# Kernel tuning notes

Measured on AMD Instinct MI355X. Metric: run time of the kernel, lower is better.

The kernel has to match this reference:

```python
import jax, jax.numpy as jnp
import numpy as np

NUM_HEADS = 32
NUM_KV_HEADS = 8
HEAD_DIM = 128
SCALE = 1.0 / np.sqrt(128.0)
B = 8          # num sequences
LQ = 1024 // 8 # new (query) tokens per sequence
PAGE_SIZE = 16


def setup_inputs() -> dict:
    key = jax.random.key(0)
    ks = jax.random.split(key, 5)
    q = jax.random.normal(ks[0], (B * LQ, NUM_HEADS * HEAD_DIM), dtype=jnp.float32)
    k = jax.random.normal(ks[1], (B * LQ, NUM_KV_HEADS * HEAD_DIM), dtype=jnp.float32)
    v = jax.random.normal(ks[2], (B * LQ, NUM_KV_HEADS * HEAD_DIM), dtype=jnp.float32)
    k_cache = jax.random.normal(ks[3], (1024, PAGE_SIZE, NUM_KV_HEADS, HEAD_DIM), dtype=jnp.float32)
    v_cache = jax.random.normal(ks[4], (1024, PAGE_SIZE, NUM_KV_HEADS, HEAD_DIM), dtype=jnp.float32)
    page_tables = jnp.arange(8 * 128, dtype=jnp.int64).reshape(8, 128)  # distinct pages per seq
    return {"q": q, "k": k, "v": v, "k_cache": k_cache, "v_cache": v_cache,
            "page_tables": page_tables, "ctx_len": 2048, "block_size": 32}


def reference(q, k, v, k_cache, v_cache, page_tables, ctx_len, block_size):
    nh, nkvh, hd = NUM_HEADS, NUM_KV_HEADS, HEAD_DIM
    group = nh // nkvh
    # split flat token dim into [B, Lq]
    qs = q.reshape(B, LQ, nh, hd)
    k_new = k.reshape(B, LQ, nkvh, hd)
    v_new = v.reshape(B, LQ, nkvh, hd)
    # paged gather of cached context: [B, n_pages, P, nkvh, hd] -> [B, ctx_len, nkvh, hd]
    k_ctx = k_cache[page_tables].reshape(B, ctx_len, nkvh, hd)
    v_ctx = v_cache[page_tables].reshape(B, ctx_len, nkvh, hd)
    k_full = jnp.concatenate([k_ctx, k_new], axis=1)  # [B, ctx_len+Lq, nkvh, hd]
    v_full = jnp.concatenate([v_ctx, v_new], axis=1)
    # GQA: repeat kv heads to match query heads (repeat_interleave over head dim)
    k_rep = jnp.repeat(k_full, group, axis=2)  # [B, K, nh, hd]
    v_rep = jnp.repeat(v_full, group, axis=2)
    scores = jnp.einsum('bqhd,bkhd->bhqk', qs, k_rep) * SCALE  # [B, nh, Lq, K]
    # diffusion block-causal mask over the new-token region; cache region fully visible
    qi = jnp.arange(LQ)
    abs_q = ctx_len + qi
    abs_k_new = ctx_len + jnp.arange(LQ)
    block_ends = (abs_q // block_size + 1) * block_size
    new_mask = abs_k_new[None, :] < block_ends[:, None]            # [Lq, Lq]
    cache_mask = jnp.ones((LQ, ctx_len), dtype=bool)
    mask = jnp.concatenate([cache_mask, new_mask], axis=1)         # [Lq, ctx_len+Lq]
    neg = jnp.finfo(scores.dtype).min
    scores = jnp.where(mask[None, None, :, :], scores, neg)
    probs = jax.nn.softmax(scores, axis=-1)
    out = jnp.einsum('bhqk,bkhd->bqhd', probs, v_rep)  # [B, Lq, nh, hd]
    return out.reshape(B * LQ, nh * hd).astype(q.dtype)
```

## Files before the change

### kernel.cpp

```cpp
#include <hip/hip_runtime.h>
#include <math.h>

#define NH 32
#define NKVH 8
#define GRP 4
#define HD 128
#define LQB 128
#define PTSTRIDE 128
#define KVROW (NKVH * HD)
#define QK_SCALE 0.08838834764831845f

typedef __attribute__((ext_vector_type(8))) __bf16 bf16x8;
typedef __attribute__((ext_vector_type(4))) __bf16 bf16x4;
typedef __attribute__((ext_vector_type(4))) float f32x4;

#define KS_BYTES 8192
#define VT_BYTES 10240
#define KS_OFF(b) ((b) * KS_BYTES)
#define VT_OFF(b) (2 * KS_BYTES + (b) * VT_BYTES)

static __device__ __forceinline__ bf16x8 cvt8s(const float* __restrict__ p, float s) {
    const f32x4 a = *reinterpret_cast<const f32x4*>(p);
    const f32x4 b = *reinterpret_cast<const f32x4*>(p + 4);
    bf16x8 r;
    r[0] = (__bf16)(a[0] * s); r[1] = (__bf16)(a[1] * s);
    r[2] = (__bf16)(a[2] * s); r[3] = (__bf16)(a[3] * s);
    r[4] = (__bf16)(b[0] * s); r[5] = (__bf16)(b[1] * s);
    r[6] = (__bf16)(b[2] * s); r[7] = (__bf16)(b[3] * s);
    return r;
}

__global__ __launch_bounds__(256, 2)
void attn_fwd(const float* __restrict__ Q,
              const float* __restrict__ Kn,
              const float* __restrict__ Vn,
              const float* __restrict__ Kc,
              const float* __restrict__ Vc,
              const int* __restrict__ PT,
              const int* __restrict__ CTX,
              float* __restrict__ O)
{
    __shared__ __align__(16) unsigned char smem[2 * KS_BYTES + 2 * VT_BYTES];

    const int ctx  = CTX[0];
    const int tid  = (int)threadIdx.x;
    const int wave = tid >> 6;
    const int lane = tid & 63;
    const int low  = lane & 15;
    const int hi   = lane >> 4;

    const int bid   = (int)blockIdx.x;
    const int kvh   = bid & 7;
    const int b     = (bid >> 3) & 7;
    const int qtile = bid >> 6;
    const int head  = kvh * GRP + wave;
    const int q0    = qtile * 16;

    const int qtok = b * LQB + q0 + low;
    const float* qrow = Q + (size_t)qtok * (NH * HD) + head * HD;

    bf16x8 qf[4];
    #pragma unroll
    for (int c = 0; c < 4; ++c) qf[c] = cvt8s(qrow + 32 * c + 8 * hi, QK_SCALE);

    f32x4 acc[8];
    #pragma unroll
    for (int c = 0; c < 8; ++c) acc[c] = (f32x4){0.f, 0.f, 0.f, 0.f};
    float mrun = -1e30f, lrun = 0.f;

    const int skey = tid >> 3;
    const int sc8  = tid & 7;
    const int kxr  = (skey & 7) << 4;
    const int vdc  = tid >> 3;
    const int vkq  = tid & 7;

    f32x4 kr[4], vr[4];

    const int nsteps = (ctx >> 5) + (q0 >> 5) + 1;

    auto issue_loads = [&](int t0) {
        {
            const float* src; size_t ro;
            const int tok = t0 + skey;
            if (t0 < ctx) {
                const int pg = PT[b * PTSTRIDE + (tok >> 4)];
                src = Kc; ro = ((size_t)pg * 16 + (tok & 15)) * KVROW + kvh * HD;
            } else {
                src = Kn; ro = (size_t)(b * LQB + tok - ctx) * KVROW + kvh * HD;
            }
            const f32x4* p = reinterpret_cast<const f32x4*>(src + ro + 16 * sc8);
            kr[0] = p[0]; kr[1] = p[1]; kr[2] = p[2]; kr[3] = p[3];
        }
        {
            const float* src; size_t ro;
            const int tok0 = t0 + 4 * vkq;
            if (t0 < ctx) {
                const int pg = PT[b * PTSTRIDE + (tok0 >> 4)];
                src = Vc; ro = ((size_t)pg * 16 + (tok0 & 15)) * KVROW + kvh * HD;
            } else {
                src = Vn; ro = (size_t)(b * LQB + tok0 - ctx) * KVROW + kvh * HD;
            }
            const float* base = src + ro + 4 * vdc;
            vr[0] = *reinterpret_cast<const f32x4*>(base);
            vr[1] = *reinterpret_cast<const f32x4*>(base + KVROW);
            vr[2] = *reinterpret_cast<const f32x4*>(base + 2 * KVROW);
            vr[3] = *reinterpret_cast<const f32x4*>(base + 3 * KVROW);
        }
    };

    auto write_tile = [&](int buf) {
        unsigned char* ks = smem + KS_OFF(buf) + skey * 256;
        bf16x8 c0, c1;
        #pragma unroll
        for (int j = 0; j < 4; ++j) {
            c0[j] = (__bf16)kr[0][j]; c0[j + 4] = (__bf16)kr[1][j];
            c1[j] = (__bf16)kr[2][j]; c1[j + 4] = (__bf16)kr[3][j];
        }
        *reinterpret_cast<bf16x8*>(ks + ((32 * sc8) ^ kxr))      = c0;
        *reinterpret_cast<bf16x8*>(ks + ((32 * sc8 + 16) ^ kxr)) = c1;
        unsigned char* vt = smem + VT_OFF(buf) + 8 * vkq;
        #pragma unroll
        for (int di = 0; di < 4; ++di) {
            bf16x4 w;
            w[0] = (__bf16)vr[0][di]; w[1] = (__bf16)vr[1][di];
            w[2] = (__bf16)vr[2][di]; w[3] = (__bf16)vr[3][di];
            *reinterpret_cast<bf16x4*>(vt + (4 * vdc + di) * 80) = w;
        }
    };

    issue_loads(0);
    write_tile(0);
    __syncthreads();

    int cur = 0;
    for (int s = 0; s < nsteps; ++s) {
        if (s + 1 < nsteps) issue_loads((s + 1) << 5);

        const unsigned char* ks = smem + KS_OFF(cur);
        const unsigned char* vt = smem + VT_OFF(cur);
        const int xr = (low & 7) << 4;

        f32x4 s0 = (f32x4){0.f, 0.f, 0.f, 0.f};
        f32x4 s1 = (f32x4){0.f, 0.f, 0.f, 0.f};
        #pragma unroll
        for (int c = 0; c < 4; ++c) {
            bf16x8 ka = *reinterpret_cast<const bf16x8*>(ks + low * 256 + ((64 * c + 16 * hi) ^ xr));
            bf16x8 kb = *reinterpret_cast<const bf16x8*>(ks + (16 + low) * 256 + ((64 * c + 16 * hi) ^ xr));
            s0 = __builtin_amdgcn_mfma_f32_16x16x32_bf16(ka, qf[c], s0, 0, 0, 0);
            s1 = __builtin_amdgcn_mfma_f32_16x16x32_bf16(kb, qf[c], s1, 0, 0, 0);
        }

        float pmax = fmaxf(fmaxf(fmaxf(s0[0], s0[1]), fmaxf(s0[2], s0[3])),
                           fmaxf(fmaxf(s1[0], s1[1]), fmaxf(s1[2], s1[3])));
        pmax = fmaxf(pmax, __shfl_xor(pmax, 16));
        pmax = fmaxf(pmax, __shfl_xor(pmax, 32));
        const float mnew = fmaxf(mrun, pmax);
        const float corr = __expf(mrun - mnew);
        mrun = mnew;

        float p[8];
        #pragma unroll
        for (int j = 0; j < 4; ++j) {
            p[j]     = __expf(s0[j] - mnew);
            p[j + 4] = __expf(s1[j] - mnew);
        }
        lrun = lrun * corr +
               (((p[0] + p[1]) + (p[2] + p[3])) + ((p[4] + p[5]) + (p[6] + p[7])));

        bf16x8 pf;
        #pragma unroll
        for (int j = 0; j < 8; ++j) pf[j] = (__bf16)p[j];

        #pragma unroll
        for (int c = 0; c < 8; ++c) acc[c] *= corr;

        #pragma unroll
        for (int c = 0; c < 8; ++c) {
            const unsigned char* vrow = vt + (16 * c + low) * 80 + 8 * hi;
            bf16x4 a0 = *reinterpret_cast<const bf16x4*>(vrow);
            bf16x4 a1 = *reinterpret_cast<const bf16x4*>(vrow + 32);
            bf16x8 vf;
            vf[0] = a0[0]; vf[1] = a0[1]; vf[2] = a0[2]; vf[3] = a0[3];
            vf[4] = a1[0]; vf[5] = a1[1]; vf[6] = a1[2]; vf[7] = a1[3];
            acc[c] = __builtin_amdgcn_mfma_f32_16x16x32_bf16(vf, pf, acc[c], 0, 0, 0);
        }

        if (s + 1 < nsteps) write_tile(cur ^ 1);
        __syncthreads();
        cur ^= 1;
    }

    lrun += __shfl_xor(lrun, 16);
    lrun += __shfl_xor(lrun, 32);
    const float inv = 1.0f / lrun;

    float* orow = O + (size_t)qtok * (NH * HD) + head * HD;
    #pragma unroll
    for (int c = 0; c < 8; ++c) {
        f32x4 r = acc[c] * inv;
        *reinterpret_cast<f32x4*>(orow + 16 * c + 4 * hi) = r;
    }
}

extern "C" void kernel_launch(void* const* d_in, const int* in_sizes, int n_in,
                              void* d_out, int out_size, void* d_ws, size_t ws_size,
                              hipStream_t stream) {
    const float* q  = (const float*)d_in[0];
    const float* k  = (const float*)d_in[1];
    const float* v  = (const float*)d_in[2];
    const float* kc = (const float*)d_in[3];
    const float* vc = (const float*)d_in[4];
    const int*   pt = (const int*)d_in[5];
    const int*   cx = (const int*)d_in[6];
    float* out = (float*)d_out;

    attn_fwd<<<dim3(512), dim3(256), 0, stream>>>(q, k, v, kc, vc, pt, cx, out);
}
```

Before: 273.0 us.

## Use 64-key tiles, exp2 softmax, and lazy rescaling in paged attention

```diff
diff --git a/kernel.cpp b/kernel.cpp
--- a/kernel.cpp
+++ b/kernel.cpp
@@ -9,13 +9,16 @@
 #define PTSTRIDE 128
 #define KVROW (NKVH * HD)
 #define QK_SCALE 0.08838834764831845f
+#define LOG2E 1.4426950408889634f
+#define DEFER_THR 8.0f
 
 typedef __attribute__((ext_vector_type(8))) __bf16 bf16x8;
 typedef __attribute__((ext_vector_type(4))) __bf16 bf16x4;
 typedef __attribute__((ext_vector_type(4))) float f32x4;
 
-#define KS_BYTES 8192
-#define VT_BYTES 10240
+#define KS_BYTES (64 * 256)
+#define VT_STRIDE 144
+#define VT_BYTES (128 * VT_STRIDE)
 #define KS_OFF(b) ((b) * KS_BYTES)
 #define VT_OFF(b) (2 * KS_BYTES + (b) * VT_BYTES)
 
@@ -61,70 +64,75 @@
 
     bf16x8 qf[4];
     #pragma unroll
-    for (int c = 0; c < 4; ++c) qf[c] = cvt8s(qrow + 32 * c + 8 * hi, QK_SCALE);
+    for (int c = 0; c < 4; ++c) qf[c] = cvt8s(qrow + 32 * c + 8 * hi, QK_SCALE * LOG2E);
 
     f32x4 acc[8];
     #pragma unroll
     for (int c = 0; c < 8; ++c) acc[c] = (f32x4){0.f, 0.f, 0.f, 0.f};
     float mrun = -1e30f, lrun = 0.f;
 
-    const int skey = tid >> 3;
-    const int sc8  = tid & 7;
+    const int vis    = ctx + (((q0 >> 5) + 1) << 5);
+    const int nsteps = (vis + 63) >> 6;
+
+    const int skey = tid >> 2;
+    const int scol = tid & 3;
     const int kxr  = (skey & 7) << 4;
-    const int vdc  = tid >> 3;
-    const int vkq  = tid & 7;
-
-    f32x4 kr[4], vr[4];
-
-    const int nsteps = (ctx >> 5) + (q0 >> 5) + 1;
+    const int vkq  = tid & 15;
+    const int vdc2 = tid >> 4;
+
+    f32x4 kr[8], vr[8];
 
     auto issue_loads = [&](int t0) {
         {
+            const int tok = t0 + skey;
             const float* src; size_t ro;
-            const int tok = t0 + skey;
-            if (t0 < ctx) {
+            if (tok < ctx) {
                 const int pg = PT[b * PTSTRIDE + (tok >> 4)];
                 src = Kc; ro = ((size_t)pg * 16 + (tok & 15)) * KVROW + kvh * HD;
             } else {
                 src = Kn; ro = (size_t)(b * LQB + tok - ctx) * KVROW + kvh * HD;
             }
-            const f32x4* p = reinterpret_cast<const f32x4*>(src + ro + 16 * sc8);
-            kr[0] = p[0]; kr[1] = p[1]; kr[2] = p[2]; kr[3] = p[3];
+            const f32x4* p = reinterpret_cast<const f32x4*>(src + ro + 32 * scol);
+            #pragma unroll
+            for (int i = 0; i < 8; ++i) kr[i] = p[i];
         }
         {
+            const int tok0 = t0 + 4 * vkq;
             const float* src; size_t ro;
-            const int tok0 = t0 + 4 * vkq;
-            if (t0 < ctx) {
+            if (tok0 < ctx) {
                 const int pg = PT[b * PTSTRIDE + (tok0 >> 4)];
                 src = Vc; ro = ((size_t)pg * 16 + (tok0 & 15)) * KVROW + kvh * HD;
             } else {
                 src = Vn; ro = (size_t)(b * LQB + tok0 - ctx) * KVROW + kvh * HD;
             }
-            const float* base = src + ro + 4 * vdc;
-            vr[0] = *reinterpret_cast<const f32x4*>(base);
-            vr[1] = *reinterpret_cast<const f32x4*>(base + KVROW);
-            vr[2] = *reinterpret_cast<const f32x4*>(base + 2 * KVROW);
-            vr[3] = *reinterpret_cast<const f32x4*>(base + 3 * KVROW);
+            const float* base = src + ro + 8 * vdc2;
+            #pragma unroll
+            for (int r = 0; r < 4; ++r) {
+                vr[2 * r]     = *reinterpret_cast<const f32x4*>(base + r * KVROW);
+                vr[2 * r + 1] = *reinterpret_cast<const f32x4*>(base + r * KVROW + 4);
+            }
         }
     };
 
     auto write_tile = [&](int buf) {
         unsigned char* ks = smem + KS_OFF(buf) + skey * 256;
-        bf16x8 c0, c1;
-        #pragma unroll
-        for (int j = 0; j < 4; ++j) {
-            c0[j] = (__bf16)kr[0][j]; c0[j + 4] = (__bf16)kr[1][j];
-            c1[j] = (__bf16)kr[2][j]; c1[j + 4] = (__bf16)kr[3][j];
-        }
-        *reinterpret_cast<bf16x8*>(ks + ((32 * sc8) ^ kxr))      = c0;
-        *reinterpret_cast<bf16x8*>(ks + ((32 * sc8 + 16) ^ kxr)) = c1;
+        #pragma unroll
+        for (int u = 0; u < 4; ++u) {
+            bf16x8 w;
+            #pragma unroll
+            for (int j = 0; j < 4; ++j) {
+                w[j]     = (__bf16)kr[2 * u][j];
+                w[4 + j] = (__bf16)kr[2 * u + 1][j];
+            }
+            *reinterpret_cast<bf16x8*>(ks + ((64 * scol + 16 * u) ^ kxr)) = w;
+        }
         unsigned char* vt = smem + VT_OFF(buf) + 8 * vkq;
         #pragma unroll
-        for (int di = 0; di < 4; ++di) {
+        for (int di = 0; di < 8; ++di) {
             bf16x4 w;
-            w[0] = (__bf16)vr[0][di]; w[1] = (__bf16)vr[1][di];
-            w[2] = (__bf16)vr[2][di]; w[3] = (__bf16)vr[3][di];
-            *reinterpret_cast<bf16x4*>(vt + (4 * vdc + di) * 80) = w;
+            #pragma unroll
+            for (int r = 0; r < 4; ++r) w[r] = (__bf16)vr[2 * r + (di >> 2)][di & 3];
+            *reinterpret_cast<bf16x4*>(vt + (8 * vdc2 + di) * VT_STRIDE) = w;
         }
     };
 
@@ -134,55 +142,80 @@
 
     int cur = 0;
     for (int s = 0; s < nsteps; ++s) {
-        if (s + 1 < nsteps) issue_loads((s + 1) << 5);
+        const int t0 = s << 6;
+        if (s + 1 < nsteps) issue_loads((s + 1) << 6);
 
         const unsigned char* ks = smem + KS_OFF(cur);
         const unsigned char* vt = smem + VT_OFF(cur);
         const int xr = (low & 7) << 4;
 
-        f32x4 s0 = (f32x4){0.f, 0.f, 0.f, 0.f};
-        f32x4 s1 = (f32x4){0.f, 0.f, 0.f, 0.f};
+        f32x4 sc[4];
+        #pragma unroll
+        for (int k = 0; k < 4; ++k) sc[k] = (f32x4){0.f, 0.f, 0.f, 0.f};
         #pragma unroll
         for (int c = 0; c < 4; ++c) {
-            bf16x8 ka = *reinterpret_cast<const bf16x8*>(ks + low * 256 + ((64 * c + 16 * hi) ^ xr));
-            bf16x8 kb = *reinterpret_cast<const bf16x8*>(ks + (16 + low) * 256 + ((64 * c + 16 * hi) ^ xr));
-            s0 = __builtin_amdgcn_mfma_f32_16x16x32_bf16(ka, qf[c], s0, 0, 0, 0);
-            s1 = __builtin_amdgcn_mfma_f32_16x16x32_bf16(kb, qf[c], s1, 0, 0, 0);
-        }
-
-        float pmax = fmaxf(fmaxf(fmaxf(s0[0], s0[1]), fmaxf(s0[2], s0[3])),
-                           fmaxf(fmaxf(s1[0], s1[1]), fmaxf(s1[2], s1[3])));
-        pmax = fmaxf(pmax, __shfl_xor(pmax, 16));
-        pmax = fmaxf(pmax, __shfl_xor(pmax, 32));
-        const float mnew = fmaxf(mrun, pmax);
-        const float corr = __expf(mrun - mnew);
-        mrun = mnew;
-
-        float p[8];
-        #pragma unroll
-        for (int j = 0; j < 4; ++j) {
-            p[j]     = __expf(s0[j] - mnew);
-            p[j + 4] = __expf(s1[j] - mnew);
-        }
-        lrun = lrun * corr +
-               (((p[0] + p[1]) + (p[2] + p[3])) + ((p[4] + p[5]) + (p[6] + p[7])));
-
-        bf16x8 pf;
-        #pragma unroll
-        for (int j = 0; j < 8; ++j) pf[j] = (__bf16)p[j];
-
-        #pragma unroll
-        for (int c = 0; c < 8; ++c) acc[c] *= corr;
+            #pragma unroll
+            for (int k = 0; k < 4; ++k) {
+                bf16x8 kf = *reinterpret_cast<const bf16x8*>(
+                    ks + (16 * k + low) * 256 + ((64 * c + 16 * hi) ^ xr));
+                sc[k] = __builtin_amdgcn_mfma_f32_16x16x32_bf16(kf, qf[c], sc[k], 0, 0, 0);
+            }
+        }
+
+        if (t0 + 32 >= vis) {
+            #pragma unroll
+            for (int j = 0; j < 4; ++j) { sc[2][j] = -1e30f; sc[3][j] = -1e30f; }
+        }
+
+        float pmax = sc[0][0];
+        #pragma unroll
+        for (int k = 0; k < 4; ++k)
+            #pragma unroll
+            for (int j = 0; j < 4; ++j) pmax = fmaxf(pmax, sc[k][j]);
+
+        if (!__all(pmax - mrun <= DEFER_THR)) {
+            float pm = fmaxf(pmax, __shfl_xor(pmax, 16));
+            pm = fmaxf(pm, __shfl_xor(pm, 32));
+            const float mnew = fmaxf(mrun, pm);
+            const float corr = exp2f(mrun - mnew);
+            mrun = mnew;
+            lrun *= corr;
+            #pragma unroll
+            for (int c = 0; c < 8; ++c) acc[c] *= corr;
+        }
+
+        float p[16];
+        float sum = 0.f;
+        #pragma unroll
+        for (int k = 0; k < 4; ++k)
+            #pragma unroll
+            for (int j = 0; j < 4; ++j) {
+                p[4 * k + j] = exp2f(sc[k][j] - mrun);
+                sum += p[4 * k + j];
+            }
+        lrun += sum;
+
+        bf16x8 pf[2];
+        #pragma unroll
+        for (int h = 0; h < 2; ++h)
+            #pragma unroll
+            for (int j = 0; j < 4; ++j) {
+                pf[h][j]     = (__bf16)p[8 * h + j];
+                pf[h][4 + j] = (__bf16)p[8 * h + 4 + j];
+            }
 
         #pragma unroll
         for (int c = 0; c < 8; ++c) {
-            const unsigned char* vrow = vt + (16 * c + low) * 80 + 8 * hi;
-            bf16x4 a0 = *reinterpret_cast<const bf16x4*>(vrow);
-            bf16x4 a1 = *reinterpret_cast<const bf16x4*>(vrow + 32);
-            bf16x8 vf;
-            vf[0] = a0[0]; vf[1] = a0[1]; vf[2] = a0[2]; vf[3] = a0[3];
-            vf[4] = a1[0]; vf[5] = a1[1]; vf[6] = a1[2]; vf[7] = a1[3];
-            acc[c] = __builtin_amdgcn_mfma_f32_16x16x32_bf16(vf, pf, acc[c], 0, 0, 0);
+            const unsigned char* vrow = vt + (16 * c + low) * VT_STRIDE;
+            #pragma unroll
+            for (int h = 0; h < 2; ++h) {
+                bf16x4 a0 = *reinterpret_cast<const bf16x4*>(vrow + 64 * h + 8 * hi);
+                bf16x4 a1 = *reinterpret_cast<const bf16x4*>(vrow + 64 * h + 32 + 8 * hi);
+                bf16x8 vf;
+                vf[0] = a0[0]; vf[1] = a0[1]; vf[2] = a0[2]; vf[3] = a0[3];
+                vf[4] = a1[0]; vf[5] = a1[1]; vf[6] = a1[2]; vf[7] = a1[3];
+                acc[c] = __builtin_amdgcn_mfma_f32_16x16x32_bf16(vf, pf[h], acc[c], 0, 0, 0);
+            }
         }
 
         if (s + 1 < nsteps) write_tile(cur ^ 1);
```

Measured after the change: 290.4 us. +6.4%, slower.

## Split KV range in two with combine kernel, defer softmax rescale, use exp2

Applied to the files above, without the earlier changes.

```diff
diff --git a/kernel.cpp b/kernel.cpp
--- a/kernel.cpp
+++ b/kernel.cpp
@@ -6,15 +6,20 @@
 #define GRP 4
 #define HD 128
 #define LQB 128
+#define B_SEQ 8
 #define PTSTRIDE 128
 #define KVROW (NKVH * HD)
 #define QK_SCALE 0.08838834764831845f
+#define LOG2E 1.4426950408889634f
+#define DEFER_THR 8.0f
+#define NROWS (B_SEQ * LQB * NH)
 
 typedef __attribute__((ext_vector_type(8))) __bf16 bf16x8;
 typedef __attribute__((ext_vector_type(4))) __bf16 bf16x4;
 typedef __attribute__((ext_vector_type(4))) float f32x4;
 
 #define KS_BYTES 8192
+#define VT_STRIDE 80
 #define VT_BYTES 10240
 #define KS_OFF(b) ((b) * KS_BYTES)
 #define VT_OFF(b) (2 * KS_BYTES + (b) * VT_BYTES)
@@ -30,7 +35,8 @@
     return r;
 }
 
-__global__ __launch_bounds__(256, 2)
+template<bool SPLIT>
+__global__ __launch_bounds__(256, 4)
 void attn_fwd(const float* __restrict__ Q,
               const float* __restrict__ Kn,
               const float* __restrict__ Vn,
@@ -38,7 +44,9 @@
               const float* __restrict__ Vc,
               const int* __restrict__ PT,
               const int* __restrict__ CTX,
-              float* __restrict__ O)
+              float* __restrict__ O,
+              float* __restrict__ WA,
+              float2* __restrict__ WML)
 {
     __shared__ __align__(16) unsigned char smem[2 * KS_BYTES + 2 * VT_BYTES];
 
@@ -52,7 +60,8 @@
     const int bid   = (int)blockIdx.x;
     const int kvh   = bid & 7;
     const int b     = (bid >> 3) & 7;
-    const int qtile = bid >> 6;
+    const int qtile = (bid >> 6) & 7;
+    const int sk    = SPLIT ? (bid >> 9) : 0;
     const int head  = kvh * GRP + wave;
     const int q0    = qtile * 16;
 
@@ -61,28 +70,32 @@
 
     bf16x8 qf[4];
     #pragma unroll
-    for (int c = 0; c < 4; ++c) qf[c] = cvt8s(qrow + 32 * c + 8 * hi, QK_SCALE);
+    for (int c = 0; c < 4; ++c) qf[c] = cvt8s(qrow + 32 * c + 8 * hi, QK_SCALE * LOG2E);
 
     f32x4 acc[8];
     #pragma unroll
     for (int c = 0; c < 8; ++c) acc[c] = (f32x4){0.f, 0.f, 0.f, 0.f};
     float mrun = -1e30f, lrun = 0.f;
 
+    const int vis  = ctx + (((q0 >> 5) + 1) << 5);
+    const int c0   = (ctx >> 1) & ~31;
+    const int kbeg = (SPLIT && sk) ? c0 : 0;
+    const int kend = SPLIT ? (sk ? vis : c0) : vis;
+    const int nsteps = (kend - kbeg) >> 5;
+
     const int skey = tid >> 3;
     const int sc8  = tid & 7;
-    const int kxr  = (skey & 7) << 4;
+    const int kxr  = (skey & 15) << 4;
     const int vdc  = tid >> 3;
     const int vkq  = tid & 7;
 
     f32x4 kr[4], vr[4];
 
-    const int nsteps = (ctx >> 5) + (q0 >> 5) + 1;
-
     auto issue_loads = [&](int t0) {
         {
+            const int tok = t0 + skey;
             const float* src; size_t ro;
-            const int tok = t0 + skey;
-            if (t0 < ctx) {
+            if (tok < ctx) {
                 const int pg = PT[b * PTSTRIDE + (tok >> 4)];
                 src = Kc; ro = ((size_t)pg * 16 + (tok & 15)) * KVROW + kvh * HD;
             } else {
@@ -92,9 +105,9 @@
             kr[0] = p[0]; kr[1] = p[1]; kr[2] = p[2]; kr[3] = p[3];
         }
         {
+            const int tok0 = t0 + 4 * vkq;
             const float* src; size_t ro;
-            const int tok0 = t0 + 4 * vkq;
-            if (t0 < ctx) {
+            if (tok0 < ctx) {
                 const int pg = PT[b * PTSTRIDE + (tok0 >> 4)];
                 src = Vc; ro = ((size_t)pg * 16 + (tok0 & 15)) * KVROW + kvh * HD;
             } else {
@@ -110,96 +123,128 @@
 
     auto write_tile = [&](int buf) {
         unsigned char* ks = smem + KS_OFF(buf) + skey * 256;
-        bf16x8 c0, c1;
+        bf16x8 c0w, c1w;
         #pragma unroll
         for (int j = 0; j < 4; ++j) {
-            c0[j] = (__bf16)kr[0][j]; c0[j + 4] = (__bf16)kr[1][j];
-            c1[j] = (__bf16)kr[2][j]; c1[j + 4] = (__bf16)kr[3][j];
-        }
-        *reinterpret_cast<bf16x8*>(ks + ((32 * sc8) ^ kxr))      = c0;
-        *reinterpret_cast<bf16x8*>(ks + ((32 * sc8 + 16) ^ kxr)) = c1;
+            c0w[j] = (__bf16)kr[0][j]; c0w[j + 4] = (__bf16)kr[1][j];
+            c1w[j] = (__bf16)kr[2][j]; c1w[j + 4] = (__bf16)kr[3][j];
+        }
+        *reinterpret_cast<bf16x8*>(ks + ((32 * sc8) ^ kxr))      = c0w;
+        *reinterpret_cast<bf16x8*>(ks + ((32 * sc8 + 16) ^ kxr)) = c1w;
         unsigned char* vt = smem + VT_OFF(buf) + 8 * vkq;
         #pragma unroll
         for (int di = 0; di < 4; ++di) {
             bf16x4 w;
             w[0] = (__bf16)vr[0][di]; w[1] = (__bf16)vr[1][di];
             w[2] = (__bf16)vr[2][di]; w[3] = (__bf16)vr[3][di];
-            *reinterpret_cast<bf16x4*>(vt + (4 * vdc + di) * 80) = w;
+            *reinterpret_cast<bf16x4*>(vt + (4 * vdc + di) * VT_STRIDE) = w;
         }
     };
 
-    issue_loads(0);
-    write_tile(0);
-    __syncthreads();
-
-    int cur = 0;
-    for (int s = 0; s < nsteps; ++s) {
-        if (s + 1 < nsteps) issue_loads((s + 1) << 5);
-
-        const unsigned char* ks = smem + KS_OFF(cur);
-        const unsigned char* vt = smem + VT_OFF(cur);
-        const int xr = (low & 7) << 4;
-
-        f32x4 s0 = (f32x4){0.f, 0.f, 0.f, 0.f};
-        f32x4 s1 = (f32x4){0.f, 0.f, 0.f, 0.f};
-        #pragma unroll
-        for (int c = 0; c < 4; ++c) {
-            bf16x8 ka = *reinterpret_cast<const bf16x8*>(ks + low * 256 + ((64 * c + 16 * hi) ^ xr));
-            bf16x8 kb = *reinterpret_cast<const bf16x8*>(ks + (16 + low) * 256 + ((64 * c + 16 * hi) ^ xr));
-            s0 = __builtin_amdgcn_mfma_f32_16x16x32_bf16(ka, qf[c], s0, 0, 0, 0);
-            s1 = __builtin_amdgcn_mfma_f32_16x16x32_bf16(kb, qf[c], s1, 0, 0, 0);
-        }
-
-        float pmax = fmaxf(fmaxf(fmaxf(s0[0], s0[1]), fmaxf(s0[2], s0[3])),
-                           fmaxf(fmaxf(s1[0], s1[1]), fmaxf(s1[2], s1[3])));
-        pmax = fmaxf(pmax, __shfl_xor(pmax, 16));
-        pmax = fmaxf(pmax, __shfl_xor(pmax, 32));
-        const float mnew = fmaxf(mrun, pmax);
-        const float corr = __expf(mrun - mnew);
-        mrun = mnew;
-
-        float p[8];
-        #pragma unroll
-        for (int j = 0; j < 4; ++j) {
-            p[j]     = __expf(s0[j] - mnew);
-            p[j + 4] = __expf(s1[j] - mnew);
-        }
-        lrun = lrun * corr +
-               (((p[0] + p[1]) + (p[2] + p[3])) + ((p[4] + p[5]) + (p[6] + p[7])));
-
-        bf16x8 pf;
-        #pragma unroll
-        for (int j = 0; j < 8; ++j) pf[j] = (__bf16)p[j];
-
-        #pragma unroll
-        for (int c = 0; c < 8; ++c) acc[c] *= corr;
-
-        #pragma unroll
-        for (int c = 0; c < 8; ++c) {
-            const unsigned char* vrow = vt + (16 * c + low) * 80 + 8 * hi;
-            bf16x4 a0 = *reinterpret_cast<const bf16x4*>(vrow);
-            bf16x4 a1 = *reinterpret_cast<const bf16x4*>(vrow + 32);
-            bf16x8 vf;
-            vf[0] = a0[0]; vf[1] = a0[1]; vf[2] = a0[2]; vf[3] = a0[3];
-            vf[4] = a1[0]; vf[5] = a1[1]; vf[6] = a1[2]; vf[7] = a1[3];
-            acc[c] = __builtin_amdgcn_mfma_f32_16x16x32_bf16(vf, pf, acc[c], 0, 0, 0);
-        }
-
-        if (s + 1 < nsteps) write_tile(cur ^ 1);
+    if (nsteps > 0) {
+        issue_loads(kbeg);
+        write_tile(0);
         __syncthreads();
-        cur ^= 1;
+
+        int cur = 0;
+        for (int s = 0; s < nsteps; ++s) {
+            if (s + 1 < nsteps) issue_loads(kbeg + ((s + 1) << 5));
+
+            const unsigned char* ks = smem + KS_OFF(cur);
+            const unsigned char* vt = smem + VT_OFF(cur);
+            const int xr = low << 4;
+
+            f32x4 s0 = (f32x4){0.f, 0.f, 0.f, 0.f};
+            f32x4 s1 = (f32x4){0.f, 0.f, 0.f, 0.f};
+            #pragma unroll
+            for (int c = 0; c < 4; ++c) {
+                bf16x8 ka = *reinterpret_cast<const bf16x8*>(ks + low * 256 + ((64 * c + 16 * hi) ^ xr));
+                bf16x8 kb = *reinterpret_cast<const bf16x8*>(ks + (16 + low) * 256 + ((64 * c + 16 * hi) ^ xr));
+                s0 = __builtin_amdgcn_mfma_f32_16x16x32_bf16(ka, qf[c], s0, 0, 0, 0);
+                s1 = __builtin_amdgcn_mfma_f32_16x16x32_bf16(kb, qf[c], s1, 0, 0, 0);
+            }
+
+            float pmax = fmaxf(fmaxf(fmaxf(s0[0], s0[1]), fmaxf(s0[2], s0[3])),
+                               fmaxf(fmaxf(s1[0], s1[1]), fmaxf(s1[2], s1[3])));
+
+            if (!__all(pmax - mrun <= DEFER_THR)) {
+                float pm = fmaxf(pmax, __shfl_xor(pmax, 16));
+                pm = fmaxf(pm, __shfl_xor(pm, 32));
+                const float mnew = fmaxf(mrun, pm);
+                const float corr = exp2f(mrun - mnew);
+                mrun = mnew;
+                lrun *= corr;
+                #pragma unroll
+                for (int c = 0; c < 8; ++c) acc[c] *= corr;
+            }
+
+            float p[8];
+            #pragma unroll
+            for (int j = 0; j < 4; ++j) {
+                p[j]     = exp2f(s0[j] - mrun);
+                p[j + 4] = exp2f(s1[j] - mrun);
+            }
+            lrun += (((p[0] + p[1]) + (p[2] + p[3])) + ((p[4] + p[5]) + (p[6] + p[7])));
+
+            bf16x8 pf;
+            #pragma unroll
+            for (int j = 0; j < 8; ++j) pf[j] = (__bf16)p[j];
+
+            #pragma unroll
+            for (int c = 0; c < 8; ++c) {
+                const unsigned char* vrow = vt + (16 * c + low) * VT_STRIDE + 8 * hi;
+                bf16x4 a0 = *reinterpret_cast<const bf16x4*>(vrow);
+                bf16x4 a1 = *reinterpret_cast<const bf16x4*>(vrow + 32);
+                bf16x8 vf;
+                vf[0] = a0[0]; vf[1] = a0[1]; vf[2] = a0[2]; vf[3] = a0[3];
+                vf[4] = a1[0]; vf[5] = a1[1]; vf[6] = a1[2]; vf[7] = a1[3];
+                acc[c] = __builtin_amdgcn_mfma_f32_16x16x32_bf16(vf, pf, acc[c], 0, 0, 0);
+            }
+
+            if (s + 1 < nsteps) write_tile(cur ^ 1);
+            __syncthreads();
+            cur ^= 1;
+        }
     }
 
     lrun += __shfl_xor(lrun, 16);
     lrun += __shfl_xor(lrun, 32);
-    const float inv = 1.0f / lrun;
-
-    float* orow = O + (size_t)qtok * (NH * HD) + head * HD;
-    #pragma unroll
-    for (int c = 0; c < 8; ++c) {
-        f32x4 r = acc[c] * inv;
-        *reinterpret_cast<f32x4*>(orow + 16 * c + 4 * hi) = r;
+
+    const int r = qtok * NH + head;
+    if (SPLIT) {
+        float* oa = WA + ((size_t)sk * NROWS + r) * HD;
+        #pragma unroll
+        for (int c = 0; c < 8; ++c)
+            *reinterpret_cast<f32x4*>(oa + 16 * c + 4 * hi) = acc[c];
+        if (hi == 0) WML[sk * NROWS + r] = make_float2(mrun, lrun);
+    } else {
+        const float inv = 1.0f / lrun;
+        float* orow = O + (size_t)r * HD;
+        #pragma unroll
+        for (int c = 0; c < 8; ++c) {
+            f32x4 v = acc[c] * inv;
+            *reinterpret_cast<f32x4*>(orow + 16 * c + 4 * hi) = v;
+        }
     }
+}
+
+__global__ __launch_bounds__(256)
+void combine(const float* __restrict__ WA, const float2* __restrict__ WML,
+             float* __restrict__ O)
+{
+    const int idx = (int)blockIdx.x * 256 + (int)threadIdx.x;
+    const int r  = idx >> 5;
+    const int dq = idx & 31;
+    const float2 ml0 = WML[r];
+    const float2 ml1 = WML[NROWS + r];
+    const float M  = fmaxf(ml0.x, ml1.x);
+    const float e0 = exp2f(ml0.x - M);
+    const float e1 = exp2f(ml1.x - M);
+    const float inv = 1.0f / (ml0.y * e0 + ml1.y * e1);
+    const f32x4 a0 = *reinterpret_cast<const f32x4*>(WA + (size_t)r * HD + 4 * dq);
+    const f32x4 a1 = *reinterpret_cast<const f32x4*>(WA + ((size_t)NROWS + r) * HD + 4 * dq);
+    f32x4 o = (a0 * e0 + a1 * e1) * inv;
+    *reinterpret_cast<f32x4*>(O + (size_t)r * HD + 4 * dq) = o;
 }
 
 extern "C" void kernel_launch(void* const* d_in, const int* in_sizes, int n_in,
@@ -214,5 +259,16 @@
     const int*   cx = (const int*)d_in[6];
     float* out = (float*)d_out;
 
-    attn_fwd<<<dim3(512), dim3(256), 0, stream>>>(q, k, v, kc, vc, pt, cx, out);
-}
+    const size_t wa_bytes = (size_t)2 * NROWS * HD * sizeof(float);
+    const size_t needed   = wa_bytes + (size_t)2 * NROWS * sizeof(float2);
+
+    if (ws_size >= needed) {
+        float*  wa  = (float*)d_ws;
+        float2* wml = (float2*)((char*)d_ws + wa_bytes);
+        attn_fwd<true><<<dim3(1024), dim3(256), 0, stream>>>(q, k, v, kc, vc, pt, cx, out, wa, wml);
+        combine<<<dim3(NROWS * 32 / 256), dim3(256), 0, stream>>>(wa, wml, out);
+    } else {
+        attn_fwd<false><<<dim3(512), dim3(256), 0, stream>>>(q, k, v, kc, vc, pt, cx, out,
+                                                             nullptr, nullptr);
+    }
+}
```

After: 271.5 us. No clear change (-0.5%).
